# Kernel optimization log

Hardware: AMD Instinct MI355X
Metric: run time of the kernel (lower is better)

Reference implementation:

```python
import jax, jax.numpy as jnp
import numpy as np

D_MODEL, SEQ, D_HEAD, N_HEAD, D_MLP = 1024, 2048, 64, 16, 4096
BATCH = 2
LN_EPS = 1e-5


def layer_norm(x, gamma, beta):
    mu = jnp.mean(x, axis=-1, keepdims=True)
    var = jnp.mean(jnp.square(x - mu), axis=-1, keepdims=True)
    return (x - mu) * jax.lax.rsqrt(var + LN_EPS) * gamma + beta


def setup_inputs() -> dict:
    key = jax.random.key(0)
    ks = jax.random.split(key, 10)
    s = 1.0 / np.sqrt(D_MODEL)
    x = jax.random.normal(ks[0], (BATCH, SEQ, D_MODEL), dtype=jnp.float32)
    # per-head Q/K/V projections, stacked: [H, d_model, d_head]
    wq = jax.random.uniform(ks[1], (N_HEAD, D_MODEL, D_HEAD), jnp.float32, -s, s)
    wk = jax.random.uniform(ks[2], (N_HEAD, D_MODEL, D_HEAD), jnp.float32, -s, s)
    wv = jax.random.uniform(ks[3], (N_HEAD, D_MODEL, D_HEAD), jnp.float32, -s, s)
    wo = jax.random.uniform(ks[4], (N_HEAD * D_HEAD, D_MODEL), jnp.float32, -s, s)
    sm = 1.0 / np.sqrt(D_MLP)
    w_in = jax.random.uniform(ks[5], (D_MODEL, D_MLP), jnp.float32, -s, s)
    b_in = jax.random.uniform(ks[6], (D_MLP,), jnp.float32, -s, s)
    w_out = jax.random.uniform(ks[7], (D_MLP, D_MODEL), jnp.float32, -sm, sm)
    b_out = jax.random.uniform(ks[8], (D_MODEL,), jnp.float32, -sm, sm)
    g1 = jnp.ones((D_MODEL,), jnp.float32)
    bt1 = jnp.zeros((D_MODEL,), jnp.float32)
    g2 = jnp.ones((D_MODEL,), jnp.float32)
    bt2 = jnp.zeros((D_MODEL,), jnp.float32)
    return {"x": x, "wq": wq, "wk": wk, "wv": wv, "wo": wo,
            "w_in": w_in, "b_in": b_in, "w_out": w_out, "b_out": b_out,
            "g1": g1, "bt1": bt1, "g2": g2, "bt2": bt2}


def reference(x, wq, wk, wv, wo, w_in, b_in, w_out, b_out, g1, bt1, g2, bt2):
    B, S, D = x.shape
    # multi-head attention (all heads batched)
    q = jnp.einsum('bsd,hde->bhse', x, wq)  # [B,H,S,dh]
    k = jnp.einsum('bsd,hde->bhse', x, wk)
    v = jnp.einsum('bsd,hde->bhse', x, wv)
    scores = jnp.einsum('bhie,bhje->bhij', q, k) / np.sqrt(D_HEAD)
    causal = jnp.tril(jnp.ones((S, S), dtype=bool))
    scores = jnp.where(causal, scores, -jnp.inf)
    attn = jax.nn.softmax(scores, axis=-1)
    head_out = jnp.einsum('bhij,bhje->bhie', attn, v)  # [B,H,S,dh]
    # concat heads in order (head 0 first) -> [B,S,H*dh]
    head_out = jnp.transpose(head_out, (0, 2, 1, 3)).reshape(B, S, N_HEAD * D_HEAD)
    x = x + layer_norm(head_out @ wo, g1, bt1)
    mlp = jax.nn.relu(x @ w_in + b_in) @ w_out + b_out
    x = x + layer_norm(mlp, g2, bt2)
    return x
```

## Files before the change

### kernel.cpp

```cpp
#include <hip/hip_runtime.h>
#include <hip/hip_bf16.h>
#include <math.h>

#define DM 1024
#define SEQ 2048
#define DH 64
#define NH 16
#define DMLP 4096
#define BATCH 2
#define ROWS (BATCH*SEQ)

typedef __attribute__((ext_vector_type(4))) float f32x4;
typedef __attribute__((ext_vector_type(8))) short bf16x8;
typedef __attribute__((ext_vector_type(4))) unsigned int u32x4;

__device__ __forceinline__ void gl2lds16(const __hip_bfloat16* g, __hip_bfloat16* l) {
  __builtin_amdgcn_global_load_lds(
      (const __attribute__((address_space(1))) void*)g,
      (__attribute__((address_space(3))) void*)l, 16, 0, 0);
}

__device__ __forceinline__ float bfu2f(unsigned short u) {
  union { unsigned int i; float f; } cvt;
  cvt.i = ((unsigned int)u) << 16;
  return cvt.f;
}

__device__ __forceinline__ unsigned short f2bu(float f) {
  __hip_bfloat16 h = __float2bfloat16(f);
  return *reinterpret_cast<unsigned short*>(&h);
}

template<int K, int KS, int OUT_BF16, int BIAS, int RELU, int VOUT>
__global__ __launch_bounds__(512) void gemm256(
    const __hip_bfloat16* __restrict__ A,
    const __hip_bfloat16* __restrict__ BT,
    float* __restrict__ Cf,
    __hip_bfloat16* __restrict__ Cb,
    const float* __restrict__ bias,
    __hip_bfloat16* __restrict__ vt,
    int N, long long zs1, long long zs2)
{
  constexpr int NT = KS / 64;
  static_assert(NT >= 2, "pipeline needs >=2 K-tiles");
  __shared__ __align__(16) __hip_bfloat16 As[2][16384];
  __shared__ __align__(16) __hip_bfloat16 Bs[2][16384];
  const int t    = threadIdx.x;
  const int wave = t >> 6;
  const int lane = t & 63;
  const int col  = lane & 15;
  const int quad = lane >> 4;
  const int m0 = blockIdx.x * 256;
  const int n0 = blockIdx.y * 256;
  const int kz = (int)blockIdx.z * KS;
  const int wm = (wave >> 2) * 128;
  const int wn = (wave & 3) * 64;

  const int tr = t >> 3;
  const int tc = (t & 7) ^ (tr & 7);
  const __hip_bfloat16* gA = A  + (size_t)(m0 + tr) * K + kz + tc * 8;
  const __hip_bfloat16* gB = BT + (size_t)(n0 + tr) * K + kz + tc * 8;

  const int sw  = col & 7;
  const int ao0 = ((quad)     ^ sw) * 8;
  const int ao1 = ((4 + quad) ^ sw) * 8;

  f32x4 acc[8][4] = {};

#define STAGE_A(h, u) do {                                                     \
    gl2lds16(gA + (size_t)(h)*128*K + (u)*64,                                  \
             &As[(u)&1][(h)*8192 + wave*512]);                                 \
    gl2lds16(gA + (size_t)(h)*128*K + (u)*64 + (size_t)64*K,                   \
             &As[(u)&1][(h)*8192 + 4096 + wave*512]);                          \
  } while (0)
#define STAGE_B(h, u) do {                                                     \
    gl2lds16(gB + (size_t)(h)*128*K + (u)*64,                                  \
             &Bs[(u)&1][(h)*8192 + wave*512]);                                 \
    gl2lds16(gB + (size_t)(h)*128*K + (u)*64 + (size_t)64*K,                   \
             &Bs[(u)&1][(h)*8192 + 4096 + wave*512]);                          \
  } while (0)
#define LOAD_A(base) do { _Pragma("unroll")                                    \
    for (int i = 0; i < 4; ++i) {                                              \
      af[i][0] = *(const bf16x8*)(pA + (base) + i*1024 + ao0);                 \
      af[i][1] = *(const bf16x8*)(pA + (base) + i*1024 + ao1);                 \
    } } while (0)
#define LOAD_BX(arr, base) do { _Pragma("unroll")                              \
    for (int j = 0; j < 2; ++j) {                                              \
      arr[j][0] = *(const bf16x8*)(pB + (base) + j*1024 + ao0);                \
      arr[j][1] = *(const bf16x8*)(pB + (base) + j*1024 + ao1);                \
    } } while (0)
#define PHASE_TAIL(MB, NB, BARR) do {                                          \
    asm volatile("s_barrier" ::: "memory");                                    \
    asm volatile("s_waitcnt lgkmcnt(0)" ::: "memory");                         \
    __builtin_amdgcn_s_setprio(1);                                             \
    _Pragma("unroll")                                                          \
    for (int kk = 0; kk < 2; ++kk)                                             \
      _Pragma("unroll")                                                        \
      for (int i = 0; i < 4; ++i)                                              \
        _Pragma("unroll")                                                      \
        for (int j = 0; j < 2; ++j)                                            \
          acc[(MB)+i][(NB)+j] = __builtin_amdgcn_mfma_f32_16x16x32_bf16(       \
              af[i][kk], BARR[j][kk], acc[(MB)+i][(NB)+j], 0, 0, 0);           \
    __builtin_amdgcn_s_setprio(0);                                             \
    asm volatile("s_barrier" ::: "memory");                                    \
  } while (0)

  STAGE_A(0, 0); STAGE_B(0, 0); STAGE_A(1, 0); STAGE_B(1, 0);
  STAGE_A(0, 1); STAGE_B(0, 1); STAGE_A(1, 1); STAGE_B(1, 1);
  asm volatile("s_waitcnt vmcnt(8)" ::: "memory");
  asm volatile("s_barrier" ::: "memory");

  #pragma unroll 2
  for (int u = 0; u < NT; ++u) {
    const __hip_bfloat16* pA = As[u & 1] + (wm + col) * 64;
    const __hip_bfloat16* pB = Bs[u & 1] + (wn + col) * 64;
    const bool s2 = (u + 2 < NT);
    bf16x8 af[4][2], bl[2][2], bh[2][2];

    LOAD_A(0);
    LOAD_BX(bl, 0);
    PHASE_TAIL(0, 0, bl);

    LOAD_BX(bh, 2048);
    PHASE_TAIL(0, 2, bh);

    LOAD_A(4096);
    if (s2) { STAGE_B(0, u + 2); STAGE_B(1, u + 2); }
    PHASE_TAIL(4, 2, bh);

    if (s2) {
      STAGE_A(0, u + 2); STAGE_A(1, u + 2);
      asm volatile("s_waitcnt vmcnt(8)" ::: "memory");
    } else {
      asm volatile("s_waitcnt vmcnt(0)" ::: "memory");
    }
    PHASE_TAIL(4, 0, bl);
  }
#undef STAGE_A
#undef STAGE_B
#undef LOAD_A
#undef LOAD_BX
#undef PHASE_TAIL

  if (VOUT && n0 >= 2048) {
    const int b = m0 >> 11;
    #pragma unroll
    for (int mi = 0; mi < 8; ++mi) {
      #pragma unroll
      for (int ni = 0; ni < 4; ++ni) {
        const int cn = n0 + wn + ni*16 + col;
        const int vc = cn - 2048;
        const int hh = vc >> 6, e = vc & 63;
        const int cm = m0 + wm + mi*16 + quad*4;
        const int s  = cm & 2047;
        ushort4 o = { f2bu(acc[mi][ni][0]), f2bu(acc[mi][ni][1]),
                      f2bu(acc[mi][ni][2]), f2bu(acc[mi][ni][3]) };
        *(ushort4*)&vt[((size_t)((b*16 + hh)*64 + e))*SEQ + s] = o;
      }
    }
    return;
  }

  const size_t zoff = (size_t)(blockIdx.z & 1) * (size_t)zs1
                    + (size_t)(blockIdx.z >> 1) * (size_t)zs2;
  __hip_bfloat16* Cbz = Cb + zoff;
  float*          Cfz = Cf + zoff;
  #pragma unroll
  for (int mi = 0; mi < 8; ++mi) {
    #pragma unroll
    for (int ni = 0; ni < 4; ++ni) {
      const int cn = n0 + wn + ni*16 + col;
      float bv = 0.f;
      if (BIAS) bv = bias[cn];
      #pragma unroll
      for (int r = 0; r < 4; ++r) {
        const int cm = m0 + wm + mi*16 + quad*4 + r;
        float v = acc[mi][ni][r];
        if (BIAS) v += bv;
        if (RELU) v = fmaxf(v, 0.f);
        if (OUT_BF16) Cbz[(size_t)cm * N + cn] = __float2bfloat16(v);
        else          Cfz[(size_t)cm * N + cn] = v;
      }
    }
  }
}

template<int KS, int SPLIT, int OUT_BF16, int BIAS, int RELU>
__global__ __launch_bounds__(256) void gemm128(
    const __hip_bfloat16* __restrict__ A,
    const __hip_bfloat16* __restrict__ BT,
    float* __restrict__ Cf,
    __hip_bfloat16* __restrict__ Cb,
    const float* __restrict__ bias,
    int N, int K, long long zstride)
{
  constexpr int NT = KS / 64;
  static_assert(NT >= 2, "pipeline needs >=2 K-tiles");
  __shared__ __align__(16) __hip_bfloat16 As[2][8192];
  __shared__ __align__(16) __hip_bfloat16 Bs[2][8192];
  const int t    = threadIdx.x;
  const int wave = t >> 6;
  const int lane = t & 63;
  const int col  = lane & 15;
  const int quad = lane >> 4;
  const int m0 = blockIdx.x * 128;
  const int n0 = blockIdx.y * 128;
  const int kz = (SPLIT > 1) ? (int)blockIdx.z * KS : 0;
  const int wm = (wave >> 1) * 64;
  const int wn = (wave & 1) * 64;

  const int tr = t >> 3;
  const int tc = (t & 7) ^ (tr & 7);
  const __hip_bfloat16* gA = A  + (size_t)(m0 + tr) * K + kz + tc * 8;
  const __hip_bfloat16* gB = BT + (size_t)(n0 + tr) * K + kz + tc * 8;

  const int sw  = col & 7;
  const int ao0 = ((quad)     ^ sw) * 8;
  const int ao1 = ((4 + quad) ^ sw) * 8;

  f32x4 acc[4][4] = {};

#define SA(u) do { _Pragma("unroll")                                           \
    for (int q = 0; q < 4; ++q)                                                \
      gl2lds16(gA + (size_t)(q*32)*K + (u)*64,                                 \
               &As[(u)&1][q*2048 + wave*512]);                                 \
  } while (0)
#define SB(u) do { _Pragma("unroll")                                           \
    for (int q = 0; q < 4; ++q)                                                \
      gl2lds16(gB + (size_t)(q*32)*K + (u)*64,                                 \
               &Bs[(u)&1][q*2048 + wave*512]);                                 \
  } while (0)

  SA(0); SB(0); SA(1);

  #pragma unroll 2
  for (int v = 0; v < NT; ++v) {
    const __hip_bfloat16* pA = As[v & 1] + (wm + col) * 64;
    const __hip_bfloat16* pB = Bs[v & 1] + (wn + col) * 64;
    bf16x8 af[4][2], bf[4][2];

    if (v + 1 < NT) {
      SB(v + 1);
      asm volatile("s_waitcnt vmcnt(8)" ::: "memory");
    } else {
      asm volatile("s_waitcnt vmcnt(0)" ::: "memory");
    }
    asm volatile("s_barrier" ::: "memory");
    #pragma unroll
    for (int i = 0; i < 4; ++i) {
      af[i][0] = *(const bf16x8*)(pA + i*1024 + ao0);
      af[i][1] = *(const bf16x8*)(pA + i*1024 + ao1);
    }
    #pragma unroll
    for (int j = 0; j < 2; ++j) {
      bf[j][0] = *(const bf16x8*)(pB + j*1024 + ao0);
      bf[j][1] = *(const bf16x8*)(pB + j*1024 + ao1);
    }
    asm volatile("s_waitcnt lgkmcnt(0)" ::: "memory");
    __builtin_amdgcn_s_setprio(1);
    #pragma unroll
    for (int kk = 0; kk < 2; ++kk)
      #pragma unroll
      for (int i = 0; i < 4; ++i)
        #pragma unroll
        for (int j = 0; j < 2; ++j)
          acc[i][j] = __builtin_amdgcn_mfma_f32_16x16x32_bf16(
              af[i][kk], bf[j][kk], acc[i][j], 0, 0, 0);
    __builtin_amdgcn_s_setprio(0);
    asm volatile("s_barrier" ::: "memory");

    if (v + 2 < NT) SA(v + 2);
    #pragma unroll
    for (int j = 2; j < 4; ++j) {
      bf[j][0] = *(const bf16x8*)(pB + j*1024 + ao0);
      bf[j][1] = *(const bf16x8*)(pB + j*1024 + ao1);
    }
    asm volatile("s_waitcnt lgkmcnt(0)" ::: "memory");
    __builtin_amdgcn_s_setprio(1);
    #pragma unroll
    for (int kk = 0; kk < 2; ++kk)
      #pragma unroll
      for (int i = 0; i < 4; ++i)
        #pragma unroll
        for (int j = 2; j < 4; ++j)
          acc[i][j] = __builtin_amdgcn_mfma_f32_16x16x32_bf16(
              af[i][kk], bf[j][kk], acc[i][j], 0, 0, 0);
    __builtin_amdgcn_s_setprio(0);
    asm volatile("s_barrier" ::: "memory");
  }
#undef SA
#undef SB

  float*          Cfz = (SPLIT > 1) ? (Cf + (size_t)blockIdx.z * zstride) : Cf;
  __hip_bfloat16* Cbz = (SPLIT > 1) ? (Cb + (size_t)blockIdx.z * zstride) : Cb;
  #pragma unroll
  for (int i = 0; i < 4; ++i) {
    #pragma unroll
    for (int j = 0; j < 4; ++j) {
      const int cn = n0 + wn + j*16 + col;
      float bv = 0.f;
      if (BIAS) bv = bias[cn];
      #pragma unroll
      for (int r = 0; r < 4; ++r) {
        const int cm = m0 + wm + i*16 + quad*4 + r;
        float v = acc[i][j][r];
        if (BIAS) v += bv;
        if (RELU) v = fmaxf(v, 0.f);
        if (OUT_BF16) Cbz[(size_t)cm * N + cn] = __float2bfloat16(v);
        else          Cfz[(size_t)cm * N + cn] = v;
      }
    }
  }
}

__global__ __launch_bounds__(256) void attn_kernel(
    const __hip_bfloat16* __restrict__ qkv,
    const __hip_bfloat16* __restrict__ vt,
    __hip_bfloat16* __restrict__ aout,
    __hip_bfloat16* __restrict__ opart,
    float* __restrict__ lpart)
{
  __shared__ __align__(16) __hip_bfloat16 Ks[2][64*64];
  __shared__ __align__(16) __hip_bfloat16 Vts[2][64*64];

  const int bh = blockIdx.x, b = bh >> 4, h = bh & 15;
  const int t = threadIdx.x, wave = t >> 6, lane = t & 63;
  const int col = lane & 15, quad = lane >> 4;
  const float SC = 0.125f * 1.44269504f;

  const int r0  = t >> 3;
  const int cs0 = (t & 7) ^ (r0 & 7);
  const int pk0 = ((r0 >> 4) & 1)*32 + ((r0 >> 2) & 3)*8 + (r0 & 3);
  const __hip_bfloat16* kbase = qkv + (size_t)b*SEQ*3072 + 1024 + h*64;
  const __hip_bfloat16* vbase = vt + (size_t)bh*64*SEQ;

#define KISSUE(j0, buf) do {                                                      \
    gl2lds16(kbase + (size_t)((j0) + pk0    )*3072 + cs0*8, &Ks[buf][wave*512]);  \
    gl2lds16(kbase + (size_t)((j0) + pk0 + 4)*3072 + cs0*8, &Ks[buf][2048 + wave*512]); \
  } while (0)
#define VISSUE(j0, buf) do {                                                      \
    gl2lds16(vbase + (size_t)r0*SEQ        + (j0) + cs0*8,  &Vts[buf][wave*512]); \
    gl2lds16(vbase + (size_t)(32 + r0)*SEQ + (j0) + cs0*8,  &Vts[buf][2048 + wave*512]); \
  } while (0)

  const int y = (int)blockIdx.y;
  int c, tl;
  if (y < 16)      { c = 0; tl = 15 - y; }
  else if (y < 28) { c = 1; tl = 31 - y; }
  else if (y < 36) { c = 2; tl = 43 - y; }
  else             { c = 3; tl = 51 - y; }
  const int jbeg = c * 8;
  const int njt  = 2*tl + 2;
  const int jend = min(jbeg + 8, njt);

  const int i0 = tl * 128;
  const int iw = i0 + wave*32;

  bf16x8 aq[2][2];
  #pragma unroll
  for (int ib = 0; ib < 2; ib++)
    #pragma unroll
    for (int kk = 0; kk < 2; kk++)
      aq[ib][kk] = *(const bf16x8*)&qkv[((size_t)(b*SEQ + iw + ib*16 + col))*3072 + h*64 + kk*32 + quad*8];

  f32x4 O[4][2] = {};
  float lsum[2] = {0.f, 0.f};

  KISSUE(jbeg * 64, 0);
  VISSUE(jbeg * 64, 0);
  for (int jt = jbeg; jt < jend; jt++) {
    const int cur = (jt - jbeg) & 1;
    const int j0 = jt * 64;
    const bool pf = (jt + 1 < jend);
    asm volatile("s_barrier" ::: "memory");
    if (pf) {
      KISSUE(j0 + 64, cur ^ 1);
      VISSUE(j0 + 64, cur ^ 1);
      asm volatile("s_waitcnt vmcnt(4)" ::: "memory");
    } else {
      asm volatile("s_waitcnt vmcnt(0)" ::: "memory");
    }

    f32x4 S[4][2] = {};
    __builtin_amdgcn_s_setprio(1);
    #pragma unroll
    for (int kk = 0; kk < 2; kk++) {
      const int sl = ((kk*4 + quad) ^ (col & 7)) * 8;
      #pragma unroll
      for (int jl = 0; jl < 4; jl++) {
        bf16x8 bk = *(const bf16x8*)&Ks[cur][(jl*16 + col)*64 + sl];
        #pragma unroll
        for (int ib = 0; ib < 2; ib++)
          S[jl][ib] = __builtin_amdgcn_mfma_f32_16x16x32_bf16(bk, aq[ib][kk], S[jl][ib], 0, 0, 0);
      }
    }
    __builtin_amdgcn_s_setprio(0);

    unsigned int pw[2][4][2];
    #pragma unroll
    for (int ib = 0; ib < 2; ib++) {
      const int ig = iw + ib*16 + col;
      if (j0 + 64 > iw + ib*16) {
        #pragma unroll
        for (int jl = 0; jl < 4; jl++) {
          const int jb = j0 + (jl & 1)*32 + quad*8 + (jl >> 1)*4;
          float p[4];
          #pragma unroll
          for (int r = 0; r < 4; r++) {
            float v = __builtin_amdgcn_exp2f(S[jl][ib][r] * SC);
            if (jb + r > ig) v = 0.f;
            p[r] = v;
            lsum[ib] += v;
          }
          pw[ib][jl][0] = (unsigned int)f2bu(p[0]) | ((unsigned int)f2bu(p[1]) << 16);
          pw[ib][jl][1] = (unsigned int)f2bu(p[2]) | ((unsigned int)f2bu(p[3]) << 16);
        }
      } else {
        #pragma unroll
        for (int jl = 0; jl < 4; jl++) {
          float p[4];
          #pragma unroll
          for (int r = 0; r < 4; r++) {
            p[r] = __builtin_amdgcn_exp2f(S[jl][ib][r] * SC);
            lsum[ib] += p[r];
          }
          pw[ib][jl][0] = (unsigned int)f2bu(p[0]) | ((unsigned int)f2bu(p[1]) << 16);
          pw[ib][jl][1] = (unsigned int)f2bu(p[2]) | ((unsigned int)f2bu(p[3]) << 16);
        }
      }
    }

    __builtin_amdgcn_s_setprio(1);
    #pragma unroll
    for (int kk = 0; kk < 2; kk++) {
      const int sl = ((kk*4 + quad) ^ (col & 7)) * 8;
      bf16x8 ap[2];
      #pragma unroll
      for (int ib = 0; ib < 2; ib++) {
        u32x4 bu = { pw[ib][kk][0], pw[ib][kk][1], pw[ib][kk+2][0], pw[ib][kk+2][1] };
        ap[ib] = __builtin_bit_cast(bf16x8, bu);
      }
      #pragma unroll
      for (int et = 0; et < 4; et++) {
        bf16x8 bv = *(const bf16x8*)&Vts[cur][(et*16 + col)*64 + sl];
        #pragma unroll
        for (int ib = 0; ib < 2; ib++)
          O[et][ib] = __builtin_amdgcn_mfma_f32_16x16x32_bf16(bv, ap[ib], O[et][ib], 0, 0, 0);
      }
    }
    __builtin_amdgcn_s_setprio(0);
  }

  #pragma unroll
  for (int ib = 0; ib < 2; ib++) {
    float s = lsum[ib];
    s += __shfl_xor(s, 16);
    s += __shfl_xor(s, 32);
    const int m = b*SEQ + iw + ib*16 + col;
    if (tl < 4) {
      const float inv = __builtin_amdgcn_rcpf(s);
      #pragma unroll
      for (int et = 0; et < 4; et++) {
        ushort4 o = { f2bu(O[et][ib][0]*inv), f2bu(O[et][ib][1]*inv),
                      f2bu(O[et][ib][2]*inv), f2bu(O[et][ib][3]*inv) };
        *(ushort4*)&aout[(size_t)m*DM + h*64 + et*16 + quad*4] = o;
      }
    } else {
      __hip_bfloat16* op = opart + ((size_t)c*ROWS + m)*DM + h*64;
      #pragma unroll
      for (int et = 0; et < 4; et++) {
        ushort4 o = { f2bu(O[et][ib][0]), f2bu(O[et][ib][1]),
                      f2bu(O[et][ib][2]), f2bu(O[et][ib][3]) };
        *(ushort4*)&op[et*16 + quad*4] = o;
      }
      if (quad == 0) lpart[((size_t)c*ROWS + m)*16 + h] = s;
    }
  }
#undef KISSUE
#undef VISSUE
}

__global__ __launch_bounds__(256) void attn_finalize(
    const __hip_bfloat16* __restrict__ opart,
    const float* __restrict__ lpart,
    __hip_bfloat16* __restrict__ aout)
{
  const int y = blockIdx.x;
  const int b = y / 1536;
  const int rem = y % 1536;
  const int tl = 4 + (rem >> 7);
  const int rr = rem & 127;
  const int m = b*SEQ + tl*128 + rr;
  const int nch = (tl >> 2) + 1;
  const int tid = threadIdx.x;
  const int h = tid >> 4;
  float o0 = 0.f, o1 = 0.f, o2 = 0.f, o3 = 0.f, l = 0.f;
  for (int c = 0; c < nch; ++c) {
    const ushort4 v = ((const ushort4*)(opart + ((size_t)c*ROWS + m)*DM))[tid];
    o0 += bfu2f(v.x); o1 += bfu2f(v.y); o2 += bfu2f(v.z); o3 += bfu2f(v.w);
    l  += lpart[((size_t)c*ROWS + m)*16 + h];
  }
  const float inv = __builtin_amdgcn_rcpf(l);
  __hip_bfloat16* p = aout + (size_t)m*DM + tid*4;
  p[0] = __float2bfloat16(o0 * inv);
  p[1] = __float2bfloat16(o1 * inv);
  p[2] = __float2bfloat16(o2 * inv);
  p[3] = __float2bfloat16(o3 * inv);
}

__global__ __launch_bounds__(256) void ln_res2(
    const __hip_bfloat16* __restrict__ y0,
    const __hip_bfloat16* __restrict__ y1,
    const float* __restrict__ xres,
    float* __restrict__ xout,
    __hip_bfloat16* __restrict__ bout,
    const float* __restrict__ gamma,
    const float* __restrict__ beta)
{
  const int row = blockIdx.x;
  const int t = threadIdx.x;
  const size_t off = (size_t)row*DM;
  const ushort4 a = ((const ushort4*)(y0 + off))[t];
  const ushort4 b = ((const ushort4*)(y1 + off))[t];
  float4 v;
  v.x = bfu2f(a.x) + bfu2f(b.x);
  v.y = bfu2f(a.y) + bfu2f(b.y);
  v.z = bfu2f(a.z) + bfu2f(b.z);
  v.w = bfu2f(a.w) + bfu2f(b.w);
  float s  = v.x + v.y + v.z + v.w;
  float sq = v.x*v.x + v.y*v.y + v.z*v.z + v.w*v.w;
  #pragma unroll
  for (int o = 32; o > 0; o >>= 1) {
    s  += __shfl_down(s, o);
    sq += __shfl_down(sq, o);
  }
  __shared__ float red[8];
  const int wave = t >> 6, lane = t & 63;
  if (lane == 0) { red[wave] = s; red[4 + wave] = sq; }
  __syncthreads();
  s  = red[0] + red[1] + red[2] + red[3];
  sq = red[4] + red[5] + red[6] + red[7];
  const float mu   = s * (1.f/DM);
  const float var  = sq * (1.f/DM) - mu*mu;
  const float rstd = rsqrtf(var + 1e-5f);
  const float4 g  = ((const float4*)gamma)[t];
  const float4 bt = ((const float4*)beta)[t];
  const float4 xr = ((const float4*)(xres + off))[t];
  float4 o;
  o.x = (v.x - mu)*rstd*g.x + bt.x + xr.x;
  o.y = (v.y - mu)*rstd*g.y + bt.y + xr.y;
  o.z = (v.z - mu)*rstd*g.z + bt.z + xr.z;
  o.w = (v.w - mu)*rstd*g.w + bt.w + xr.w;
  ((float4*)(xout + off))[t] = o;
  __hip_bfloat16* bp = bout + off + t*4;
  bp[0] = __float2bfloat16(o.x);
  bp[1] = __float2bfloat16(o.y);
  bp[2] = __float2bfloat16(o.z);
  bp[3] = __float2bfloat16(o.w);
}

__global__ __launch_bounds__(256) void ln_res4(
    const __hip_bfloat16* __restrict__ y0,
    const __hip_bfloat16* __restrict__ y1,
    const __hip_bfloat16* __restrict__ y2,
    const __hip_bfloat16* __restrict__ y3,
    const float* __restrict__ bias,
    const float* __restrict__ xres,
    float* __restrict__ xout,
    const float* __restrict__ gamma,
    const float* __restrict__ beta)
{
  const int row = blockIdx.x;
  const int t = threadIdx.x;
  const size_t off = (size_t)row*DM;
  const ushort4 a = ((const ushort4*)(y0 + off))[t];
  const ushort4 b = ((const ushort4*)(y1 + off))[t];
  const ushort4 cc = ((const ushort4*)(y2 + off))[t];
  const ushort4 d = ((const ushort4*)(y3 + off))[t];
  const float4 bv = ((const float4*)bias)[t];
  float4 v;
  v.x = bfu2f(a.x) + bfu2f(b.x) + bfu2f(cc.x) + bfu2f(d.x) + bv.x;
  v.y = bfu2f(a.y) + bfu2f(b.y) + bfu2f(cc.y) + bfu2f(d.y) + bv.y;
  v.z = bfu2f(a.z) + bfu2f(b.z) + bfu2f(cc.z) + bfu2f(d.z) + bv.z;
  v.w = bfu2f(a.w) + bfu2f(b.w) + bfu2f(cc.w) + bfu2f(d.w) + bv.w;
  float s  = v.x + v.y + v.z + v.w;
  float sq = v.x*v.x + v.y*v.y + v.z*v.z + v.w*v.w;
  #pragma unroll
  for (int o = 32; o > 0; o >>= 1) {
    s  += __shfl_down(s, o);
    sq += __shfl_down(sq, o);
  }
  __shared__ float red[8];
  const int wave = t >> 6, lane = t & 63;
  if (lane == 0) { red[wave] = s; red[4 + wave] = sq; }
  __syncthreads();
  s  = red[0] + red[1] + red[2] + red[3];
  sq = red[4] + red[5] + red[6] + red[7];
  const float mu   = s * (1.f/DM);
  const float var  = sq * (1.f/DM) - mu*mu;
  const float rstd = rsqrtf(var + 1e-5f);
  const float4 g  = ((const float4*)gamma)[t];
  const float4 bt = ((const float4*)beta)[t];
  const float4 xr = ((const float4*)(xres + off))[t];
  float4 o;
  o.x = (v.x - mu)*rstd*g.x + bt.x + xr.x;
  o.y = (v.y - mu)*rstd*g.y + bt.y + xr.y;
  o.z = (v.z - mu)*rstd*g.z + bt.z + xr.z;
  o.w = (v.w - mu)*rstd*g.w + bt.w + xr.w;
  ((float4*)(xout + off))[t] = o;
}

__global__ __launch_bounds__(256) void prep_all(
    const float* __restrict__ x,
    const float* __restrict__ wq, const float* __restrict__ wk,
    const float* __restrict__ wv,
    const float* __restrict__ wo, const float* __restrict__ w_in,
    const float* __restrict__ w_out,
    __hip_bfloat16* __restrict__ xb, __hip_bfloat16* __restrict__ wqkvT,
    __hip_bfloat16* __restrict__ woT, __hip_bfloat16* __restrict__ w_inT,
    __hip_bfloat16* __restrict__ w_outT)
{
  int id = blockIdx.x;
  if (id < 4096) {
    const int i = id*256 + threadIdx.x;
    const float4 v = ((const float4*)x)[i];
    xb[i*4+0] = __float2bfloat16(v.x);
    xb[i*4+1] = __float2bfloat16(v.y);
    xb[i*4+2] = __float2bfloat16(v.z);
    xb[i*4+3] = __float2bfloat16(v.w);
    return;
  }
  id -= 4096;
  __shared__ float tile[32][33];
  const int tx = threadIdx.x & 31, ty = threadIdx.x >> 5;
  if (id < 3072) {
    const int z = id >> 6, rem = id & 63;
    const int k0 = (rem >> 1) * 32, n0 = (rem & 1) * 32;
    const int op = z >> 4, hh = z & 15;
    const float* srcs[3] = { wq, wk, wv };
    const float* s = srcs[op] + (size_t)hh * DM * DH;
    __hip_bfloat16* d = wqkvT + (size_t)z * DH * DM;
    for (int i = ty; i < 32; i += 8)
      tile[i][tx] = s[(size_t)(k0+i)*DH + n0 + tx];
    __syncthreads();
    for (int i = ty; i < 32; i += 8)
      d[(size_t)(n0+i)*DM + k0 + tx] = __float2bfloat16(tile[tx][i]);
    return;
  }
  id -= 3072;
  const float* s; __hip_bfloat16* d; int K, N, bx;
  if (id < 1024)      { s = wo;    d = woT;    K = DM;   N = DM;   bx = 32;  }
  else if (id < 5120) { id -= 1024; s = w_in;  d = w_inT;  K = DM;   N = DMLP; bx = 128; }
  else                { id -= 5120; s = w_out; d = w_outT; K = DMLP; N = DM;   bx = 32;  }
  const int n0 = (id % bx) * 32, k0 = (id / bx) * 32;
  for (int i = ty; i < 32; i += 8)
    tile[i][tx] = s[(size_t)(k0+i)*N + n0 + tx];
  __syncthreads();
  for (int i = ty; i < 32; i += 8)
    d[(size_t)(n0+i)*K + k0 + tx] = __float2bfloat16(tile[tx][i]);
}

extern "C" void kernel_launch(void* const* d_in, const int* in_sizes, int n_in,
                              void* d_out, int out_size, void* d_ws, size_t ws_size,
                              hipStream_t stream)
{
  const float* x     = (const float*)d_in[0];
  const float* wq    = (const float*)d_in[1];
  const float* wk    = (const float*)d_in[2];
  const float* wv    = (const float*)d_in[3];
  const float* wo    = (const float*)d_in[4];
  const float* w_in  = (const float*)d_in[5];
  const float* b_in  = (const float*)d_in[6];
  const float* w_out = (const float*)d_in[7];
  const float* b_out = (const float*)d_in[8];
  const float* g1    = (const float*)d_in[9];
  const float* bt1   = (const float*)d_in[10];
  const float* g2    = (const float*)d_in[11];
  const float* bt2   = (const float*)d_in[12];
  float* out = (float*)d_out;

  char* ws = (char*)d_ws;
  __hip_bfloat16* xb     = (__hip_bfloat16*)(ws + 0);
  __hip_bfloat16* wqkvT  = (__hip_bfloat16*)(ws + 8388608);
  __hip_bfloat16* woT    = (__hip_bfloat16*)(ws + 14680064);
  __hip_bfloat16* w_inT  = (__hip_bfloat16*)(ws + 16777216);
  __hip_bfloat16* w_outT = (__hip_bfloat16*)(ws + 25165824);
  __hip_bfloat16* qkvb   = (__hip_bfloat16*)(ws + 33554432);
  __hip_bfloat16* vtb    = (__hip_bfloat16*)(ws + 58720256);
  __hip_bfloat16* attn_o = (__hip_bfloat16*)(ws + 0);
  __hip_bfloat16* opart  = (__hip_bfloat16*)(ws + 67108864);
  float*          lpart  = (float*)(ws + 100663296);
  __hip_bfloat16* pp0    = (__hip_bfloat16*)(ws + 33554432);
  __hip_bfloat16* pp1    = (__hip_bfloat16*)(ws + 41943040);
  float*          x1     = (float*)(ws + 75497472);
  __hip_bfloat16* x1b    = (__hip_bfloat16*)(ws + 92274688);
  __hip_bfloat16* hbuf   = (__hip_bfloat16*)(ws + 33554432);
  __hip_bfloat16* mp0    = (__hip_bfloat16*)(ws + 0);
  __hip_bfloat16* mp1    = (__hip_bfloat16*)(ws + 8388608);
  __hip_bfloat16* mp2    = (__hip_bfloat16*)(ws + 92274688);
  __hip_bfloat16* mp3    = (__hip_bfloat16*)(ws + 100663296);

  const long long PPZ  = 8388608LL / 2;
  const long long MZS1 = 8388608LL / 2;
  const long long MZS2 = 92274688LL / 2;

  prep_all<<<16384, 256, 0, stream>>>(x, wq, wk, wv, wo, w_in, w_out,
                                      xb, wqkvT, woT, w_inT, w_outT);

  gemm256<DM,DM,1,0,0,1><<<dim3(ROWS/256, 3072/256, 1), 512, 0, stream>>>(xb, wqkvT, nullptr, qkvb, nullptr, vtb, 3072, 0, 0);
  attn_kernel<<<dim3(BATCH*NH, 40), 256, 0, stream>>>(qkvb, vtb, attn_o, opart, lpart);
  attn_finalize<<<3072, 256, 0, stream>>>(opart, lpart, attn_o);
  gemm128<512,2,1,0,0><<<dim3(ROWS/128, DM/128, 2), 256, 0, stream>>>(attn_o, woT, nullptr, pp0, nullptr, DM, DM, PPZ);
  ln_res2<<<ROWS, 256, 0, stream>>>(pp0, pp1, x, x1, x1b, g1, bt1);
  gemm256<DM,DM,1,1,1,0><<<dim3(ROWS/256, DMLP/256, 1), 512, 0, stream>>>(x1b, w_inT, nullptr, hbuf, b_in, nullptr, DMLP, 0, 0);
  gemm256<DMLP,DM,1,0,0,0><<<dim3(ROWS/256, DM/256, 4), 512, 0, stream>>>(hbuf, w_outT, nullptr, mp0, nullptr, nullptr, DM, MZS1, MZS2);
  ln_res4<<<ROWS, 256, 0, stream>>>(mp0, mp1, mp2, mp3, b_out, x1, out, g2, bt2);
}
```

Before: 209.9 us.

## Overlap wo/w_in/w_out weight transposes with the QKV projection GEMM

Moves the fp32-to-bf16 transposes of wo, w_in and w_out out of the prep kernel and into extra blocks appended to the QKV GEMM launch, flattening its grid to 1D (192 GEMM tiles plus 4608 transpose blocks). Each extra 512-thread block handles two 32x32 tiles, using the GEMM's shared memory as scratch. The aim is to run this memory-bound conversion alongside the compute-bound GEMM and shrink the prep kernel. The tradeoff is that transpose blocks reserve the GEMM's large shared-memory allocation, which limits how many fit on a CU, and block scheduling order decides how much overlap actually happens.

New measurement: 219.8 us. 1.05x slower.

```diff
diff --git a/kernel.cpp b/kernel.cpp
--- a/kernel.cpp
+++ b/kernel.cpp
@@ -39,19 +39,45 @@
     __hip_bfloat16* __restrict__ Cb,
     const float* __restrict__ bias,
     __hip_bfloat16* __restrict__ vt,
+    const float* __restrict__ wo, const float* __restrict__ w_in,
+    const float* __restrict__ w_out,
+    __hip_bfloat16* __restrict__ woT, __hip_bfloat16* __restrict__ w_inT,
+    __hip_bfloat16* __restrict__ w_outT,
     int N, long long zs1, long long zs2)
 {
   constexpr int NT = KS / 64;
   static_assert(NT >= 2, "pipeline needs >=2 K-tiles");
   __shared__ __align__(16) __hip_bfloat16 As[2][16384];
   __shared__ __align__(16) __hip_bfloat16 Bs[2][16384];
+  const int bidx = (int)blockIdx.x;
+
+  if (VOUT && bidx >= 192) {
+    float* tbase = (float*)&As[0][0];
+    const int half = threadIdx.x >> 8;
+    const int tt   = threadIdx.x & 255;
+    int tl = (bidx - 192) * 2 + half;
+    const float* s; __hip_bfloat16* dd; int KK, NN, bxw;
+    if (tl < 1024)      { s = wo;    dd = woT;    KK = DM;   NN = DM;   bxw = 32;  }
+    else if (tl < 5120) { tl -= 1024; s = w_in;  dd = w_inT;  KK = DM;   NN = DMLP; bxw = 128; }
+    else                { tl -= 5120; s = w_out; dd = w_outT; KK = DMLP; NN = DM;   bxw = 32;  }
+    const int n0t = (tl % bxw) * 32, k0t = (tl / bxw) * 32;
+    const int tx = tt & 31, ty = tt >> 5;
+    float* T = tbase + half * 1056;
+    for (int i = ty; i < 32; i += 8)
+      T[i*33 + tx] = s[(size_t)(k0t+i)*NN + n0t + tx];
+    __syncthreads();
+    for (int i = ty; i < 32; i += 8)
+      dd[(size_t)(n0t+i)*KK + k0t + tx] = __float2bfloat16(T[tx*33 + i]);
+    return;
+  }
+
   const int t    = threadIdx.x;
   const int wave = t >> 6;
   const int lane = t & 63;
   const int col  = lane & 15;
   const int quad = lane >> 4;
-  const int m0 = blockIdx.x * 256;
-  const int n0 = blockIdx.y * 256;
+  const int m0 = (VOUT ? (bidx & 15) : (int)blockIdx.x) * 256;
+  const int n0 = (VOUT ? (bidx >> 4) : (int)blockIdx.y) * 256;
   const int kz = (int)blockIdx.z * KS;
   const int wm = (wave >> 2) * 128;
   const int wn = (wave & 3) * 64;
@@ -614,11 +640,7 @@
     const float* __restrict__ x,
     const float* __restrict__ wq, const float* __restrict__ wk,
     const float* __restrict__ wv,
-    const float* __restrict__ wo, const float* __restrict__ w_in,
-    const float* __restrict__ w_out,
-    __hip_bfloat16* __restrict__ xb, __hip_bfloat16* __restrict__ wqkvT,
-    __hip_bfloat16* __restrict__ woT, __hip_bfloat16* __restrict__ w_inT,
-    __hip_bfloat16* __restrict__ w_outT)
+    __hip_bfloat16* __restrict__ xb, __hip_bfloat16* __restrict__ wqkvT)
 {
   int id = blockIdx.x;
   if (id < 4096) {
@@ -633,31 +655,17 @@
   id -= 4096;
   __shared__ float tile[32][33];
   const int tx = threadIdx.x & 31, ty = threadIdx.x >> 5;
-  if (id < 3072) {
-    const int z = id >> 6, rem = id & 63;
-    const int k0 = (rem >> 1) * 32, n0 = (rem & 1) * 32;
-    const int op = z >> 4, hh = z & 15;
-    const float* srcs[3] = { wq, wk, wv };
-    const float* s = srcs[op] + (size_t)hh * DM * DH;
-    __hip_bfloat16* d = wqkvT + (size_t)z * DH * DM;
-    for (int i = ty; i < 32; i += 8)
-      tile[i][tx] = s[(size_t)(k0+i)*DH + n0 + tx];
-    __syncthreads();
-    for (int i = ty; i < 32; i += 8)
-      d[(size_t)(n0+i)*DM + k0 + tx] = __float2bfloat16(tile[tx][i]);
-    return;
-  }
-  id -= 3072;
-  const float* s; __hip_bfloat16* d; int K, N, bx;
-  if (id < 1024)      { s = wo;    d = woT;    K = DM;   N = DM;   bx = 32;  }
-  else if (id < 5120) { id -= 1024; s = w_in;  d = w_inT;  K = DM;   N = DMLP; bx = 128; }
-  else                { id -= 5120; s = w_out; d = w_outT; K = DMLP; N = DM;   bx = 32;  }
-  const int n0 = (id % bx) * 32, k0 = (id / bx) * 32;
+  const int z = id >> 6, rem = id & 63;
+  const int k0 = (rem >> 1) * 32, n0 = (rem & 1) * 32;
+  const int op = z >> 4, hh = z & 15;
+  const float* srcs[3] = { wq, wk, wv };
+  const float* s = srcs[op] + (size_t)hh * DM * DH;
+  __hip_bfloat16* d = wqkvT + (size_t)z * DH * DM;
   for (int i = ty; i < 32; i += 8)
-    tile[i][tx] = s[(size_t)(k0+i)*N + n0 + tx];
+    tile[i][tx] = s[(size_t)(k0+i)*DH + n0 + tx];
   __syncthreads();
   for (int i = ty; i < 32; i += 8)
-    d[(size_t)(n0+i)*K + k0 + tx] = __float2bfloat16(tile[tx][i]);
+    d[(size_t)(n0+i)*DM + k0 + tx] = __float2bfloat16(tile[tx][i]);
 }
 
 extern "C" void kernel_launch(void* const* d_in, const int* in_sizes, int n_in,
@@ -704,15 +712,20 @@
   const long long MZS1 = 8388608LL / 2;
   const long long MZS2 = 92274688LL / 2;
 
-  prep_all<<<16384, 256, 0, stream>>>(x, wq, wk, wv, wo, w_in, w_out,
-                                      xb, wqkvT, woT, w_inT, w_outT);
-
-  gemm256<DM,DM,1,0,0,1><<<dim3(ROWS/256, 3072/256, 1), 512, 0, stream>>>(xb, wqkvT, nullptr, qkvb, nullptr, vtb, 3072, 0, 0);
+  prep_all<<<7168, 256, 0, stream>>>(x, wq, wk, wv, xb, wqkvT);
+
+  gemm256<DM,DM,1,0,0,1><<<dim3(4800, 1, 1), 512, 0, stream>>>(
+      xb, wqkvT, nullptr, qkvb, nullptr, vtb,
+      wo, w_in, w_out, woT, w_inT, w_outT, 3072, 0, 0);
   attn_kernel<<<dim3(BATCH*NH, 40), 256, 0, stream>>>(qkvb, vtb, attn_o, opart, lpart);
   attn_finalize<<<3072, 256, 0, stream>>>(opart, lpart, attn_o);
   gemm128<512,2,1,0,0><<<dim3(ROWS/128, DM/128, 2), 256, 0, stream>>>(attn_o, woT, nullptr, pp0, nullptr, DM, DM, PPZ);
   ln_res2<<<ROWS, 256, 0, stream>>>(pp0, pp1, x, x1, x1b, g1, bt1);
-  gemm256<DM,DM,1,1,1,0><<<dim3(ROWS/256, DMLP/256, 1), 512, 0, stream>>>(x1b, w_inT, nullptr, hbuf, b_in, nullptr, DMLP, 0, 0);
-  gemm256<DMLP,DM,1,0,0,0><<<dim3(ROWS/256, DM/256, 4), 512, 0, stream>>>(hbuf, w_outT, nullptr, mp0, nullptr, nullptr, DM, MZS1, MZS2);
+  gemm256<DM,DM,1,1,1,0><<<dim3(ROWS/256, DMLP/256, 1), 512, 0, stream>>>(
+      x1b, w_inT, nullptr, hbuf, b_in, nullptr,
+      nullptr, nullptr, nullptr, nullptr, nullptr, nullptr, DMLP, 0, 0);
+  gemm256<DMLP,DM,1,0,0,0><<<dim3(ROWS/256, DM/256, 4), 512, 0, stream>>>(
+      hbuf, w_outT, nullptr, mp0, nullptr, nullptr,
+      nullptr, nullptr, nullptr, nullptr, nullptr, nullptr, DM, MZS1, MZS2);
   ln_res4<<<ROWS, 256, 0, stream>>>(mp0, mp1, mp2, mp3, b_out, x1, out, g2, bt2);
 }
```
